# Optimization experiments

Hardware: AMD Instinct MI355X
Metric: run time of the kernel (lower is better)

The kernel has to match this reference:

```python
import jax, jax.numpy as jnp
import numpy as np

EPS = 1e-5

def _conv1x1(x, w, b):
    # x: [B,C,...], w: [O,C], b: [O]
    y = jnp.einsum('oc,bc...->bo...', w, x)
    return y + b.reshape((1, -1) + (1,) * (x.ndim - 2))

def _bn(x, g, be, m, v):
    # inference-mode BatchNorm with running stats (PyTorch eps=1e-5)
    s = (1, -1) + (1,) * (x.ndim - 2)
    return (x - m.reshape(s)) * (g.reshape(s) / jnp.sqrt(v.reshape(s) + EPS)) + be.reshape(s)

def _patches3x3(x):
    # F.unfold(kernel=3, pad=1, stride=1, dil=1): [B,C,H,W] -> [B,C,9,H,W], row-major kernel order
    B, C, H, W = x.shape
    xp = jnp.pad(x, ((0, 0), (0, 0), (1, 1), (1, 1)))
    return jnp.stack([xp[:, :, ky:ky + H, kx:kx + W] for ky in range(3) for kx in range(3)], axis=2)

def setup_inputs() -> dict:
    key = jax.random.key(0)
    ks = jax.random.split(key, 40)
    B, Cin, H, W = 4, 16, 192, 192
    Cm = 64  # mlp[-1]
    d = {}
    d['x'] = jax.random.normal(ks[0], (B, Cin, H, W), jnp.float32)
    d['group_mask'] = jnp.ones((B, 1, H, W), jnp.float32)
    d['group_xyz'] = jax.random.normal(ks[1], (B, 3, 9, H, W), jnp.float32)
    def bnp(k, c):
        k1, k2, k3, k4 = jax.random.split(k, 4)
        return (1.0 + 0.1 * jax.random.normal(k1, (c,)), 0.1 * jax.random.normal(k2, (c,)),
                0.1 * jax.random.normal(k3, (c,)), 0.5 + jax.random.uniform(k4, (c,)))
    d['w0'] = 0.1 * jax.random.normal(ks[2], (Cm, Cin)); d['b0'] = 0.01 * jax.random.normal(ks[3], (Cm,))
    d['g0'], d['beta0'], d['m0'], d['v0'] = bnp(ks[4], Cm)
    wn_dims = [(8, 3), (8, 8), (16, 8)]
    for i, (o, c) in enumerate(wn_dims):
        d[f'wn_w{i}'] = 0.3 * jax.random.normal(ks[5 + 3 * i], (o, c))
        d[f'wn_b{i}'] = 0.01 * jax.random.normal(ks[6 + 3 * i], (o,))
        d[f'wn_g{i}'], d[f'wn_beta{i}'], d[f'wn_m{i}'], d[f'wn_v{i}'] = bnp(ks[7 + 3 * i], o)
    d['lw'] = 0.05 * jax.random.normal(ks[20], (Cm, 16 * Cm)); d['lb'] = 0.01 * jax.random.normal(ks[21], (Cm,))
    d['lg'], d['lbeta'], d['lm'], d['lv'] = bnp(ks[22], Cm)
    return d

def reference(x, group_mask, group_xyz,
              w0, b0, g0, beta0, m0, v0,
              wn_w0, wn_b0, wn_g0, wn_beta0, wn_m0, wn_v0,
              wn_w1, wn_b1, wn_g1, wn_beta1, wn_m1, wn_v1,
              wn_w2, wn_b2, wn_g2, wn_beta2, wn_m2, wn_v2,
              lw, lb, lg, lbeta, lm, lv):
    # mlp_convs chain (single layer here)
    x = jax.nn.relu(_bn(_conv1x1(x, w0, b0), g0, beta0, m0, v0))  # [B,Cm,H,W]
    B, _, N, H, W = group_xyz.shape
    # WeightNet on local coords: [B,3,N,H*W] -> [B,16,N,H*W]
    gz = group_xyz.reshape(B, 3, N, H * W)
    for w, b, g, be, m, v in ((wn_w0, wn_b0, wn_g0, wn_beta0, wn_m0, wn_v0),
                              (wn_w1, wn_b1, wn_g1, wn_beta1, wn_m1, wn_v1),
                              (wn_w2, wn_b2, wn_g2, wn_beta2, wn_m2, wn_v2)):
        gz = jax.nn.relu(_bn(_conv1x1(gz, w, b), g, be, m, v))
    gz = gz.reshape(B, 16, N, H, W)
    p = _patches3x3(x)  # [B,Cm,9,H,W]
    C = p.shape[1]
    # per-pixel matmul: [B,H,W,C,9] @ [B,H,W,9,16] -> [B,H,W,C,16]
    out = jnp.einsum('bckhw,bokhw->bhwco', p, gz)
    out = out.reshape(B, H, W, C * 16).transpose(0, 3, 1, 2)  # [B,16*Cm,H,W]
    return jax.nn.relu(_bn(_conv1x1(out, lw, lb), lg, lbeta, lm, lv))
```

## Files before the change

kernel.cpp:

```cpp
#include <hip/hip_runtime.h>
#include <hip/hip_bf16.h>

#define HH 192
#define WW 192
#define HWPROD (192*192)
#define EPSBN 1e-5f

typedef _Float16 f16x8 __attribute__((ext_vector_type(8)));
typedef _Float16 f16x4 __attribute__((ext_vector_type(4)));
typedef _Float16 f16x2 __attribute__((ext_vector_type(2)));
typedef float f32x4 __attribute__((ext_vector_type(4)));
typedef float f32x16 __attribute__((ext_vector_type(16)));

__global__ __launch_bounds__(256) void prep_conv0_k(
                       const float* __restrict__ w0, const float* __restrict__ b0,
                       const float* __restrict__ g0, const float* __restrict__ beta0,
                       const float* __restrict__ m0, const float* __restrict__ v0,
                       const float* __restrict__ wnw0, const float* __restrict__ wnb0,
                       const float* __restrict__ wng0, const float* __restrict__ wnbe0,
                       const float* __restrict__ wnm0, const float* __restrict__ wnv0,
                       const float* __restrict__ wnw1, const float* __restrict__ wnb1,
                       const float* __restrict__ wng1, const float* __restrict__ wnbe1,
                       const float* __restrict__ wnm1, const float* __restrict__ wnv1,
                       const float* __restrict__ wnw2, const float* __restrict__ wnb2,
                       const float* __restrict__ wng2, const float* __restrict__ wnbe2,
                       const float* __restrict__ wnm2, const float* __restrict__ wnv2,
                       const float* __restrict__ lw, const float* __restrict__ lb,
                       const float* __restrict__ lg, const float* __restrict__ lbeta,
                       const float* __restrict__ lm, const float* __restrict__ lv,
                       const float* __restrict__ x,
                       _Float16* __restrict__ x1L,
                       _Float16* __restrict__ whF,
                       float* __restrict__ lbf,
                       float* __restrict__ wnP)
{
    const int tid = threadIdx.x;

    if (blockIdx.x >= 576) {
        int idx = (blockIdx.x - 576) * 256 + tid;
        if (idx < 65536) {
            int j    = idx & 7;
            int lane = (idx >> 3) & 63;
            int kg   = (idx >> 9) & 63;
            int nt   = idx >> 15;
            int k = kg * 16 + ((lane >> 5) & 1) * 8 + j;
            int n = nt * 32 + (lane & 31);
            float s = lg[n] * rsqrtf(lv[n] + EPSBN);
            whF[idx] = (_Float16)(lw[n * 1024 + k] * s);
        } else if (idx < 65600) {
            int j = idx - 65536;
            float s = lg[j] * rsqrtf(lv[j] + EPSBN);
            lbf[j] = (lb[j] - lm[j]) * s + lbeta[j];
        } else if (idx < 65848) {
            int t = idx - 65600;
            if (t < 24)       { int o = t / 3;           float s = wng0[o] * rsqrtf(wnv0[o] + EPSBN); wnP[t] = wnw0[t] * s; }
            else if (t < 32)  { int o = t - 24;          float s = wng0[o] * rsqrtf(wnv0[o] + EPSBN); wnP[t] = (wnb0[o] - wnm0[o]) * s + wnbe0[o]; }
            else if (t < 96)  { int t2 = t - 32;  int o = t2 >> 3; float s = wng1[o] * rsqrtf(wnv1[o] + EPSBN); wnP[t] = wnw1[t2] * s; }
            else if (t < 104) { int o = t - 96;          float s = wng1[o] * rsqrtf(wnv1[o] + EPSBN); wnP[t] = (wnb1[o] - wnm1[o]) * s + wnbe1[o]; }
            else if (t < 232) { int t2 = t - 104; int o = t2 >> 3; float s = wng2[o] * rsqrtf(wnv2[o] + EPSBN); wnP[t] = wnw2[t2] * s; }
            else if (t < 248) { int o = t - 232;         float s = wng2[o] * rsqrtf(wnv2[o] + EPSBN); wnP[t] = (wnb2[o] - wnm2[o]) * s + wnbe2[o]; }
        }
        return;
    }

    __shared__ float wSt[16][64];
    __shared__ float bS[64];
    for (int t = tid; t < 1024; t += 256) {
        int o = t >> 4, ci = t & 15;
        float s = g0[o] * rsqrtf(v0[o] + EPSBN);
        wSt[ci][o] = w0[t] * s;
    }
    if (tid < 64) {
        float s = g0[tid] * rsqrtf(v0[tid] + EPSBN);
        bS[tid] = (b0[tid] - m0[tid]) * s + beta0[tid];
    }
    __syncthreads();

    const int pix = blockIdx.x * 256 + tid;
    const int b = pix / HWPROD;
    const int p = pix - b * HWPROD;

    float xv[16];
#pragma unroll
    for (int cin = 0; cin < 16; cin++)
        xv[cin] = x[((size_t)b * 16 + cin) * HWPROD + p];

    _Float16* outp = x1L + (size_t)pix * 64;
#pragma unroll
    for (int co = 0; co < 64; co += 4) {
        f32x4 a = { bS[co], bS[co + 1], bS[co + 2], bS[co + 3] };
#pragma unroll
        for (int cin = 0; cin < 16; cin++) {
            float xc = xv[cin];
            a.x += wSt[cin][co + 0] * xc;
            a.y += wSt[cin][co + 1] * xc;
            a.z += wSt[cin][co + 2] * xc;
            a.w += wSt[cin][co + 3] * xc;
        }
        a.x = fmaxf(a.x, 0.f); a.y = fmaxf(a.y, 0.f);
        a.z = fmaxf(a.z, 0.f); a.w = fmaxf(a.w, 0.f);
        *(f16x4*)(outp + co) = __builtin_convertvector(a, f16x4);
    }
}

__global__ __launch_bounds__(128, 4) void pconv_main_k(const float* __restrict__ gxyz,
                                                       const _Float16* __restrict__ x1L,
                                                       const _Float16* __restrict__ whF,
                                                       const float* __restrict__ lbf,
                                                       const float* __restrict__ wnP,
                                                       float* __restrict__ out)
{
    __shared__ __align__(16) char smem[19456];
    unsigned*  xSu = reinterpret_cast<unsigned*>(smem);
    _Float16*  gzF = reinterpret_cast<_Float16*>(smem);
    float*     Cb  = reinterpret_cast<float*>(smem);

    const int tid = threadIdx.x;
    const int bid = blockIdx.x;
    const int b   = bid / (96 * 6);
    const int rem = bid % (96 * 6);
    const int hb  = rem / 6;
    const int c6  = rem % 6;
    const int h   = hb * 2;
    const int wc0 = c6 * 32;

    for (int u = tid; u < 576; u += 128) {
        int col = u & 31, rrow = (u >> 5) & 1, tap = u >> 6;
        size_t base = ((size_t)(b * 3) * 9 + tap) * HWPROD + (size_t)(h + rrow) * WW + wc0 + col;
        float z0 = gxyz[base];
        float z1 = gxyz[base + (size_t)9 * HWPROD];
        float z2 = gxyz[base + (size_t)18 * HWPROD];
        float h0[8], h1[8];
#pragma unroll
        for (int o = 0; o < 8; o++) {
            float a = wnP[24 + o] + wnP[o * 3 + 0] * z0 + wnP[o * 3 + 1] * z1 + wnP[o * 3 + 2] * z2;
            h0[o] = fmaxf(a, 0.f);
        }
#pragma unroll
        for (int o = 0; o < 8; o++) {
            float a = wnP[96 + o];
#pragma unroll
            for (int c = 0; c < 8; c++) a += wnP[32 + o * 8 + c] * h0[c];
            h1[o] = fmaxf(a, 0.f);
        }
        float g[16];
#pragma unroll
        for (int o = 0; o < 16; o++) {
            float a = wnP[232 + o];
#pragma unroll
            for (int c = 0; c < 8; c++) a += wnP[104 + o * 8 + c] * h1[c];
            g[o] = fmaxf(a, 0.f);
        }
        f16x8 lo, hi;
#pragma unroll
        for (int o = 0; o < 8; o++) { lo[o] = (_Float16)g[o]; hi[o] = (_Float16)g[o + 8]; }
        int pixb = u & 63;
        *(f16x8*)&gzF[pixb * 152 + tap * 16]     = lo;
        *(f16x8*)&gzF[pixb * 152 + tap * 16 + 8] = hi;
    }
    __syncthreads();

    const int lane = tid & 63;
    const int w    = tid >> 6;
    const int p31  = lane & 31;
    const int oh   = lane >> 5;
    const int pixb = w * 32 + p31;

    f16x2 gq2[9][4];
#pragma unroll
    for (int t = 0; t < 9; t++) {
        union { f16x8 v; f16x2 h[4]; } G;
        G.v = *(const f16x8*)&gzF[pixb * 152 + t * 16 + oh * 8];
#pragma unroll
        for (int d = 0; d < 4; d++) gq2[t][d] = G.h[d];
    }
    __syncthreads();

    for (int i = 0; i < 16; i++) {
        int u  = i * 128 + tid;
        int cq = u & 15;
        int cc = ((u >> 4) & 31) + 1;
        int rr = u >> 9;
        int hr = h + rr - 1;
        uint2 v = {0u, 0u};
        if (hr >= 0 && hr < HH)
            v = *(const uint2*)(x1L + (((size_t)b * HH + hr) * WW + wc0 + cc - 1) * 64 + cq * 4);
        xSu[(2 * cq) * 137 + rr * 34 + cc]     = v.x;
        xSu[(2 * cq + 1) * 137 + rr * 34 + cc] = v.y;
    }
    {
        int cq   = tid & 15;
        int side = (tid >> 4) & 1;
        int rr   = tid >> 5;
        int cc   = side ? 33 : 0;
        int hr = h + rr - 1;
        int wc = wc0 + cc - 1;
        uint2 v = {0u, 0u};
        if (hr >= 0 && hr < HH && wc >= 0 && wc < WW)
            v = *(const uint2*)(x1L + (((size_t)b * HH + hr) * WW + wc) * 64 + cq * 4);
        xSu[(2 * cq) * 137 + rr * 34 + cc]     = v.x;
        xSu[(2 * cq + 1) * 137 + rr * 34 + cc] = v.y;
    }
    __syncthreads();

    const f16x8* whF8 = (const f16x8*)whF;
    const unsigned* xrow = xSu + w * 34 + p31;

    f32x16 facc0, facc1;
#pragma unroll
    for (int r = 0; r < 16; r++) { facc0[r] = 0.f; facc1[r] = 0.f; }

#pragma unroll 2
    for (int cb = 0; cb < 32; cb++) {
        const int c0 = 2 * cb, c1 = 2 * cb + 1;
        const f16x8 wh00 = whF8[(0 * 64 + c0) * 64 + lane];
        const f16x8 wh01 = whF8[(1 * 64 + c0) * 64 + lane];
        const f16x8 wh10 = whF8[(0 * 64 + c1) * 64 + lane];
        const f16x8 wh11 = whF8[(1 * 64 + c1) * 64 + lane];

        union { f16x2 h2[4]; f16x8 v; } av0, av1;
#pragma unroll
        for (int d = 0; d < 4; d++) { av0.h2[d] = f16x2{0, 0}; av1.h2[d] = f16x2{0, 0}; }
        const unsigned* xr = xrow + cb * 137;
#pragma unroll
        for (int ky = 0; ky < 3; ky++) {
#pragma unroll
            for (int kx = 0; kx < 3; kx++) {
                const int t = ky * 3 + kx;
                f16x2 xq;
                { unsigned tmp = xr[ky * 34 + kx]; xq = *(f16x2*)&tmp; }
#pragma unroll
                for (int d = 0; d < 4; d++) {
                    asm("v_pk_fma_f16 %0, %1, %2, %0 op_sel:[0,0,0] op_sel_hi:[0,1,1]"
                        : "+v"(av0.h2[d]) : "v"(xq), "v"(gq2[t][d]));
                    asm("v_pk_fma_f16 %0, %1, %2, %0 op_sel:[1,0,0] op_sel_hi:[1,1,1]"
                        : "+v"(av1.h2[d]) : "v"(xq), "v"(gq2[t][d]));
                }
            }
        }
        facc0 = __builtin_amdgcn_mfma_f32_32x32x16_f16(av0.v, wh00, facc0, 0, 0, 0);
        facc1 = __builtin_amdgcn_mfma_f32_32x32x16_f16(av0.v, wh01, facc1, 0, 0, 0);
        facc0 = __builtin_amdgcn_mfma_f32_32x32x16_f16(av1.v, wh10, facc0, 0, 0, 0);
        facc1 = __builtin_amdgcn_mfma_f32_32x32x16_f16(av1.v, wh11, facc1, 0, 0, 0);
    }
    __syncthreads();

    {
        const int n0 = p31;
        const float bias0 = lbf[n0];
        const float bias1 = lbf[n0 + 32];
#pragma unroll
        for (int r = 0; r < 16; r++) {
            const int m = (r & 3) + 8 * (r >> 2) + 4 * oh;
            Cb[n0 * 67 + w * 32 + m]        = fmaxf(facc0[r] + bias0, 0.f);
            Cb[(n0 + 32) * 67 + w * 32 + m] = fmaxf(facc1[r] + bias1, 0.f);
        }
    }
    __syncthreads();
    {
        const int col = tid & 31;
        const int nq  = tid >> 5;
#pragma unroll
        for (int rr = 0; rr < 2; rr++) {
            size_t ob = ((size_t)b * 64 + nq * 16) * HWPROD + (size_t)(h + rr) * WW + wc0 + col;
#pragma unroll
            for (int i = 0; i < 16; i++)
                out[ob + (size_t)i * HWPROD] = Cb[(nq * 16 + i) * 67 + rr * 32 + col];
        }
    }
}

extern "C" void kernel_launch(void* const* d_in, const int* in_sizes, int n_in,
                              void* d_out, int out_size, void* d_ws, size_t ws_size,
                              hipStream_t stream) {
    const float* x    = (const float*)d_in[0];
    const float* gxyz = (const float*)d_in[2];

    char* ws = (char*)d_ws;
    _Float16* x1L = (_Float16*)ws;
    _Float16* whF = x1L + 9437184;
    float* lbf = (float*)(whF + 65536);
    float* wnP = lbf + 64;

    prep_conv0_k<<<838, 256, 0, stream>>>(
        (const float*)d_in[3],  (const float*)d_in[4],  (const float*)d_in[5],
        (const float*)d_in[6],  (const float*)d_in[7],  (const float*)d_in[8],
        (const float*)d_in[9],  (const float*)d_in[10], (const float*)d_in[11],
        (const float*)d_in[12], (const float*)d_in[13], (const float*)d_in[14],
        (const float*)d_in[15], (const float*)d_in[16], (const float*)d_in[17],
        (const float*)d_in[18], (const float*)d_in[19], (const float*)d_in[20],
        (const float*)d_in[21], (const float*)d_in[22], (const float*)d_in[23],
        (const float*)d_in[24], (const float*)d_in[25], (const float*)d_in[26],
        (const float*)d_in[27], (const float*)d_in[28], (const float*)d_in[29],
        (const float*)d_in[30], (const float*)d_in[31], (const float*)d_in[32],
        x, x1L, whF, lbf, wnP);

    pconv_main_k<<<4 * 96 * 6, 128, 0, stream>>>(gxyz, x1L, whF, lbf, wnP,
                                                 (float*)d_out);
}
```

Measured before the change: 215.1 us.

## Software-pipeline weight/activation loads in main loop and vectorize WeightNet over pixel pairs

The main channel loop now double-buffers the global weight fragments and the shared-memory activation taps, issuing loads for the next chunk before computing the current one. The goal is to hide global and LDS latency behind the packed-FMA and MFMA work. The WeightNet prologue now processes two adjacent pixels per thread with float2 loads and packed FMA, halving iterations and widening memory accesses. Launch bounds are relaxed from 4 to 3 waves per SIMD so the extra live registers fit. This trades occupancy for latency hiding.

```diff
diff --git a/kernel.cpp b/kernel.cpp
--- a/kernel.cpp
+++ b/kernel.cpp
@@ -10,6 +10,7 @@
 typedef _Float16 f16x4 __attribute__((ext_vector_type(4)));
 typedef _Float16 f16x2 __attribute__((ext_vector_type(2)));
 typedef float f32x4 __attribute__((ext_vector_type(4)));
+typedef float f32x2 __attribute__((ext_vector_type(2)));
 typedef float f32x16 __attribute__((ext_vector_type(16)));
 
 __global__ __launch_bounds__(256) void prep_conv0_k(
@@ -103,7 +104,7 @@
     }
 }
 
-__global__ __launch_bounds__(128, 4) void pconv_main_k(const float* __restrict__ gxyz,
+__global__ __launch_bounds__(128, 3) void pconv_main_k(const float* __restrict__ gxyz,
                                                        const _Float16* __restrict__ x1L,
                                                        const _Float16* __restrict__ whF,
                                                        const float* __restrict__ lbf,
@@ -124,39 +125,57 @@
     const int h   = hb * 2;
     const int wc0 = c6 * 32;
 
-    for (int u = tid; u < 576; u += 128) {
-        int col = u & 31, rrow = (u >> 5) & 1, tap = u >> 6;
+    for (int v = tid; v < 288; v += 128) {
+        int tap  = v >> 5;
+        int pr   = v & 31;
+        int rrow = pr >> 4;
+        int col  = (pr & 15) * 2;
+        int pixb = rrow * 32 + col;
         size_t base = ((size_t)(b * 3) * 9 + tap) * HWPROD + (size_t)(h + rrow) * WW + wc0 + col;
-        float z0 = gxyz[base];
-        float z1 = gxyz[base + (size_t)9 * HWPROD];
-        float z2 = gxyz[base + (size_t)18 * HWPROD];
-        float h0[8], h1[8];
+        f32x2 z0 = *(const f32x2*)(gxyz + base);
+        f32x2 z1 = *(const f32x2*)(gxyz + base + (size_t)9 * HWPROD);
+        f32x2 z2 = *(const f32x2*)(gxyz + base + (size_t)18 * HWPROD);
+        f32x2 h0[8], h1[8];
 #pragma unroll
         for (int o = 0; o < 8; o++) {
-            float a = wnP[24 + o] + wnP[o * 3 + 0] * z0 + wnP[o * 3 + 1] * z1 + wnP[o * 3 + 2] * z2;
-            h0[o] = fmaxf(a, 0.f);
+            float w0s = wnP[o * 3 + 0], w1s = wnP[o * 3 + 1], w2s = wnP[o * 3 + 2];
+            f32x2 a = { wnP[24 + o], wnP[24 + o] };
+            a = __builtin_elementwise_fma(f32x2{w0s, w0s}, z0, a);
+            a = __builtin_elementwise_fma(f32x2{w1s, w1s}, z1, a);
+            a = __builtin_elementwise_fma(f32x2{w2s, w2s}, z2, a);
+            h0[o] = __builtin_elementwise_max(a, f32x2{0.f, 0.f});
         }
 #pragma unroll
         for (int o = 0; o < 8; o++) {
-            float a = wnP[96 + o];
-#pragma unroll
-            for (int c = 0; c < 8; c++) a += wnP[32 + o * 8 + c] * h0[c];
-            h1[o] = fmaxf(a, 0.f);
-        }
-        float g[16];
+            f32x2 a = { wnP[96 + o], wnP[96 + o] };
+#pragma unroll
+            for (int c = 0; c < 8; c++) {
+                float ws = wnP[32 + o * 8 + c];
+                a = __builtin_elementwise_fma(f32x2{ws, ws}, h0[c], a);
+            }
+            h1[o] = __builtin_elementwise_max(a, f32x2{0.f, 0.f});
+        }
+        f32x2 g[16];
 #pragma unroll
         for (int o = 0; o < 16; o++) {
-            float a = wnP[232 + o];
-#pragma unroll
-            for (int c = 0; c < 8; c++) a += wnP[104 + o * 8 + c] * h1[c];
-            g[o] = fmaxf(a, 0.f);
-        }
-        f16x8 lo, hi;
-#pragma unroll
-        for (int o = 0; o < 8; o++) { lo[o] = (_Float16)g[o]; hi[o] = (_Float16)g[o + 8]; }
-        int pixb = u & 63;
-        *(f16x8*)&gzF[pixb * 152 + tap * 16]     = lo;
-        *(f16x8*)&gzF[pixb * 152 + tap * 16 + 8] = hi;
+            f32x2 a = { wnP[232 + o], wnP[232 + o] };
+#pragma unroll
+            for (int c = 0; c < 8; c++) {
+                float ws = wnP[104 + o * 8 + c];
+                a = __builtin_elementwise_fma(f32x2{ws, ws}, h1[c], a);
+            }
+            g[o] = __builtin_elementwise_max(a, f32x2{0.f, 0.f});
+        }
+        f16x8 lo0, hi0, lo1, hi1;
+#pragma unroll
+        for (int o = 0; o < 8; o++) {
+            lo0[o] = (_Float16)g[o][0];     hi0[o] = (_Float16)g[o + 8][0];
+            lo1[o] = (_Float16)g[o][1];     hi1[o] = (_Float16)g[o + 8][1];
+        }
+        *(f16x8*)&gzF[pixb * 152 + tap * 16]           = lo0;
+        *(f16x8*)&gzF[pixb * 152 + tap * 16 + 8]       = hi0;
+        *(f16x8*)&gzF[(pixb + 1) * 152 + tap * 16]     = lo1;
+        *(f16x8*)&gzF[(pixb + 1) * 152 + tap * 16 + 8] = hi1;
     }
     __syncthreads();
 
@@ -210,38 +229,54 @@
 #pragma unroll
     for (int r = 0; r < 16; r++) { facc0[r] = 0.f; facc1[r] = 0.f; }
 
-#pragma unroll 2
-    for (int cb = 0; cb < 32; cb++) {
-        const int c0 = 2 * cb, c1 = 2 * cb + 1;
-        const f16x8 wh00 = whF8[(0 * 64 + c0) * 64 + lane];
-        const f16x8 wh01 = whF8[(1 * 64 + c0) * 64 + lane];
-        const f16x8 wh10 = whF8[(0 * 64 + c1) * 64 + lane];
-        const f16x8 wh11 = whF8[(1 * 64 + c1) * 64 + lane];
-
+    f16x2 xqA[9], xqB[9];
+    f16x8 whA[4], whB[4];
+
+    auto LOADX = [&](f16x2 (&xq)[9], int cb) {
+        const unsigned* xr = xrow + cb * 137;
+#pragma unroll
+        for (int ky = 0; ky < 3; ky++)
+#pragma unroll
+            for (int kx = 0; kx < 3; kx++) {
+                unsigned tmp = xr[ky * 34 + kx];
+                xq[ky * 3 + kx] = *(f16x2*)&tmp;
+            }
+    };
+    auto LOADW = [&](f16x8 (&wh)[4], int cb) {
+        wh[0] = whF8[(0  + 2 * cb)     * 64 + lane];
+        wh[1] = whF8[(64 + 2 * cb)     * 64 + lane];
+        wh[2] = whF8[(0  + 2 * cb + 1) * 64 + lane];
+        wh[3] = whF8[(64 + 2 * cb + 1) * 64 + lane];
+    };
+    auto CHUNK = [&](const f16x2 (&xq)[9], const f16x8 (&wh)[4]) {
         union { f16x2 h2[4]; f16x8 v; } av0, av1;
 #pragma unroll
         for (int d = 0; d < 4; d++) { av0.h2[d] = f16x2{0, 0}; av1.h2[d] = f16x2{0, 0}; }
-        const unsigned* xr = xrow + cb * 137;
-#pragma unroll
-        for (int ky = 0; ky < 3; ky++) {
-#pragma unroll
-            for (int kx = 0; kx < 3; kx++) {
-                const int t = ky * 3 + kx;
-                f16x2 xq;
-                { unsigned tmp = xr[ky * 34 + kx]; xq = *(f16x2*)&tmp; }
-#pragma unroll
-                for (int d = 0; d < 4; d++) {
-                    asm("v_pk_fma_f16 %0, %1, %2, %0 op_sel:[0,0,0] op_sel_hi:[0,1,1]"
-                        : "+v"(av0.h2[d]) : "v"(xq), "v"(gq2[t][d]));
-                    asm("v_pk_fma_f16 %0, %1, %2, %0 op_sel:[1,0,0] op_sel_hi:[1,1,1]"
-                        : "+v"(av1.h2[d]) : "v"(xq), "v"(gq2[t][d]));
-                }
+#pragma unroll
+        for (int t = 0; t < 9; t++) {
+#pragma unroll
+            for (int d = 0; d < 4; d++) {
+                asm("v_pk_fma_f16 %0, %1, %2, %0 op_sel:[0,0,0] op_sel_hi:[0,1,1]"
+                    : "+v"(av0.h2[d]) : "v"(xq[t]), "v"(gq2[t][d]));
+                asm("v_pk_fma_f16 %0, %1, %2, %0 op_sel:[1,0,0] op_sel_hi:[1,1,1]"
+                    : "+v"(av1.h2[d]) : "v"(xq[t]), "v"(gq2[t][d]));
             }
         }
-        facc0 = __builtin_amdgcn_mfma_f32_32x32x16_f16(av0.v, wh00, facc0, 0, 0, 0);
-        facc1 = __builtin_amdgcn_mfma_f32_32x32x16_f16(av0.v, wh01, facc1, 0, 0, 0);
-        facc0 = __builtin_amdgcn_mfma_f32_32x32x16_f16(av1.v, wh10, facc0, 0, 0, 0);
-        facc1 = __builtin_amdgcn_mfma_f32_32x32x16_f16(av1.v, wh11, facc1, 0, 0, 0);
+        facc0 = __builtin_amdgcn_mfma_f32_32x32x16_f16(av0.v, wh[0], facc0, 0, 0, 0);
+        facc1 = __builtin_amdgcn_mfma_f32_32x32x16_f16(av0.v, wh[1], facc1, 0, 0, 0);
+        facc0 = __builtin_amdgcn_mfma_f32_32x32x16_f16(av1.v, wh[2], facc0, 0, 0, 0);
+        facc1 = __builtin_amdgcn_mfma_f32_32x32x16_f16(av1.v, wh[3], facc1, 0, 0, 0);
+    };
+
+    LOADW(whA, 0);
+    LOADX(xqA, 0);
+#pragma unroll 1
+    for (int cb = 0; cb < 32; cb += 2) {
+        LOADW(whB, cb + 1);
+        LOADX(xqB, cb + 1);
+        CHUNK(xqA, whA);
+        if (cb < 30) { LOADW(whA, cb + 2); LOADX(xqA, cb + 2); }
+        CHUNK(xqB, whB);
     }
     __syncthreads();
 
```

After: 225.3 us. +4.7%, slower.
